# Kernel optimization log

Hardware: AMD Instinct MI355X
Metric: run time of the kernel (lower is better)

Reference implementation:

```python
import jax, jax.numpy as jnp
import numpy as np

D = 64          # slot_dim == input_dim
K = 8           # num_slots
NUM_ITERS = 3
EPS = 1e-8      # attention renorm eps
LN_EPS = 1e-5   # torch LayerNorm default
SCALE = float(np.sqrt(D))


def _ln(x, g, b):
    m = x.mean(-1, keepdims=True)
    v = ((x - m) ** 2).mean(-1, keepdims=True)
    return (x - m) / jnp.sqrt(v + LN_EPS) * g + b


def setup_inputs() -> dict:
    key = jax.random.key(0)
    ks = jax.random.split(key, 12)
    B, N = 128, 4096
    s = 1.0 / np.sqrt(D)
    return {
        "inputs": jax.random.normal(ks[0], (B, N, D), jnp.float32),
        "noise": jax.random.normal(ks[1], (B, K, D), jnp.float32),
        "slot_mu": jax.random.normal(ks[2], (1, 1, D), jnp.float32),
        "slot_log_sigma": jnp.zeros((1, 1, D), jnp.float32),
        "Wq": jax.random.normal(ks[3], (D, D), jnp.float32) * s,
        "Wk": jax.random.normal(ks[4], (D, D), jnp.float32) * s,
        "Wv": jax.random.normal(ks[5], (D, D), jnp.float32) * s,
        "gru_wih": jax.random.normal(ks[6], (3 * D, D), jnp.float32) * s,
        "gru_whh": jax.random.normal(ks[7], (3 * D, D), jnp.float32) * s,
        "gru_bih": jnp.zeros((3 * D,), jnp.float32),
        "gru_bhh": jnp.zeros((3 * D,), jnp.float32),
        "ln_in_g": jnp.ones((D,), jnp.float32),
        "ln_in_b": jnp.zeros((D,), jnp.float32),
        "ln_s_g": jnp.ones((D,), jnp.float32),
        "ln_s_b": jnp.zeros((D,), jnp.float32),
        "mlp_ln_g": jnp.ones((D,), jnp.float32),
        "mlp_ln_b": jnp.zeros((D,), jnp.float32),
        "mlp_w1": jax.random.normal(ks[8], (4 * D, D), jnp.float32) * s,
        "mlp_b1": jnp.zeros((4 * D,), jnp.float32),
        "mlp_w2": jax.random.normal(ks[9], (D, 4 * D), jnp.float32) * (1.0 / np.sqrt(4 * D)),
        "mlp_b2": jnp.zeros((D,), jnp.float32),
    }


def reference(inputs, noise, slot_mu, slot_log_sigma, Wq, Wk, Wv,
              gru_wih, gru_whh, gru_bih, gru_bhh,
              ln_in_g, ln_in_b, ln_s_g, ln_s_b,
              mlp_ln_g, mlp_ln_b, mlp_w1, mlp_b1, mlp_w2, mlp_b2):
    x = _ln(inputs, ln_in_g, ln_in_b)          # (B, N, D)
    k = x @ Wk.T                               # (B, N, D)
    v = x @ Wv.T                               # (B, N, D)
    slots = slot_mu + jnp.exp(slot_log_sigma) * noise  # (B, K, D)
    for _ in range(NUM_ITERS):
        slots_prev = slots
        s = _ln(slots, ln_s_g, ln_s_b)
        q = s @ Wq.T                           # (B, K, D)
        attn = jnp.einsum('bkd,bnd->bkn', q, k) / SCALE
        attn = jax.nn.softmax(attn, axis=1)    # compete over slots
        attn_w = attn / (attn.sum(-1, keepdims=True) + EPS)
        updates = jnp.einsum('bkn,bnd->bkd', attn_w, v)
        # GRUCell(updates, slots_prev)
        gi = updates @ gru_wih.T + gru_bih
        gh = slots_prev @ gru_whh.T + gru_bhh
        i_r, i_z, i_n = jnp.split(gi, 3, axis=-1)
        h_r, h_z, h_n = jnp.split(gh, 3, axis=-1)
        r = jax.nn.sigmoid(i_r + h_r)
        z = jax.nn.sigmoid(i_z + h_z)
        n = jnp.tanh(i_n + r * h_n)
        slots = (1.0 - z) * n + z * slots_prev
        # residual MLP
        h = _ln(slots, mlp_ln_g, mlp_ln_b)
        slots = slots + jax.nn.relu(h @ mlp_w1.T + mlp_b1) @ mlp_w2.T + mlp_b2
    return slots
```

## Files before the change

### kernel.cpp

```cpp
#include <hip/hip_runtime.h>
#include <cstdint>

#define Bn 128
#define Nn 4096
#define Dn 64
#define Kn 8
#define PBn 8
#define NCHUNKn (Nn / PBn)
#define LN_EPSf 1e-5f
#define EPSf 1e-8f
#define LOG2Ef 1.4426950408889634f

typedef unsigned short u16x8 __attribute__((ext_vector_type(8)));

static __device__ __forceinline__ uint16_t f2bf(float f) {
    union { float f; uint32_t u; } v; v.f = f;
    return (uint16_t)((v.u + 0x7fffu + ((v.u >> 16) & 1u)) >> 16);
}
static __device__ __forceinline__ float bflo(uint32_t u) {
    union { uint32_t u; float f; } v; v.u = u << 16; return v.f;
}
static __device__ __forceinline__ float bfhi(uint32_t u) {
    union { uint32_t u; float f; } v; v.u = u & 0xffff0000u; return v.f;
}

template <int CTRL>
static __device__ __forceinline__ float dppadd(float x) {
    int p = __builtin_amdgcn_update_dpp(0, __float_as_int(x), CTRL, 0xf, 0xf, false);
    return x + __int_as_float(p);
}

__global__ __launch_bounds__(256) void kM(const float* __restrict__ Wq,
                                          const float* __restrict__ Wk,
                                          float* __restrict__ M) {
    const int idx = blockIdx.x * 256 + threadIdx.x;
    const int e = idx >> 6, f = idx & 63;
    float acc = 0.f;
#pragma unroll 8
    for (int d = 0; d < 64; ++d) acc += Wq[d * 64 + e] * Wk[d * 64 + f];
    M[idx] = acc * 0.125f * LOG2Ef;
}

__global__ __launch_bounds__(256) void kinit_qk(
    const float* __restrict__ noise, const float* __restrict__ mu,
    const float* __restrict__ ls, const float* __restrict__ M,
    float* __restrict__ slots, float* __restrict__ qk) {
    __shared__ float sraw[Kn * Dn];
    __shared__ float sln[Kn][68];
    const int t = threadIdx.x;
    const int b = blockIdx.x;

    if (t < 128) {
        const int base = (b * 128 + t) * 4;
        const int d = base & 63;
        float4 nz = *(const float4*)(noise + base);
        float4 m4 = *(const float4*)(mu + d);
        float4 s4 = *(const float4*)(ls + d);
        float4 o;
        o.x = m4.x + __expf(s4.x) * nz.x;
        o.y = m4.y + __expf(s4.y) * nz.y;
        o.z = m4.z + __expf(s4.z) * nz.z;
        o.w = m4.w + __expf(s4.w) * nz.w;
        *(float4*)(slots + base) = o;
        *(float4*)(sraw + t * 4) = o;
    }
    __syncthreads();
    if (t < 128) {
        const int row = t >> 4, l16 = t & 15;
        float4 v4 = *(const float4*)(sraw + row * 64 + l16 * 4);
        float s1 = v4.x + v4.y + v4.z + v4.w;
        float s2 = v4.x * v4.x + v4.y * v4.y + v4.z * v4.z + v4.w * v4.w;
        s1 = dppadd<0xB1>(s1); s2 = dppadd<0xB1>(s2);
        s1 = dppadd<0x4E>(s1); s2 = dppadd<0x4E>(s2);
        s1 = dppadd<0x141>(s1); s2 = dppadd<0x141>(s2);
        s1 = dppadd<0x128>(s1); s2 = dppadd<0x128>(s2);
        const float mean = s1 * (1.0f / 64.0f);
        const float var = s2 * (1.0f / 64.0f) - mean * mean;
        const float rstd = rsqrtf(var + LN_EPSf);
        const float xs[4] = {v4.x, v4.y, v4.z, v4.w};
#pragma unroll
        for (int i = 0; i < 4; ++i) sln[row][l16 * 4 + i] = (xs[i] - mean) * rstd;
    }
    __syncthreads();
    ((void)0);
}

__global__ __launch_bounds__(256) void kinit_qk_full(
    const float* __restrict__ noise, const float* __restrict__ mu,
    const float* __restrict__ ls, const float* __restrict__ M,
    const float* __restrict__ lsg, const float* __restrict__ lsb,
    float* __restrict__ slots, float* __restrict__ qk) {
    __shared__ float sraw[Kn * Dn];
    __shared__ float sln[Kn][68];
    const int t = threadIdx.x;
    const int b = blockIdx.x;

    if (t < 128) {
        const int base = (b * 128 + t) * 4;
        const int d = base & 63;
        float4 nz = *(const float4*)(noise + base);
        float4 m4 = *(const float4*)(mu + d);
        float4 s4 = *(const float4*)(ls + d);
        float4 o;
        o.x = m4.x + __expf(s4.x) * nz.x;
        o.y = m4.y + __expf(s4.y) * nz.y;
        o.z = m4.z + __expf(s4.z) * nz.z;
        o.w = m4.w + __expf(s4.w) * nz.w;
        *(float4*)(slots + base) = o;
        *(float4*)(sraw + t * 4) = o;
    }
    __syncthreads();
    if (t < 128) {
        const int row = t >> 4, l16 = t & 15;
        float4 v4 = *(const float4*)(sraw + row * 64 + l16 * 4);
        float s1 = v4.x + v4.y + v4.z + v4.w;
        float s2 = v4.x * v4.x + v4.y * v4.y + v4.z * v4.z + v4.w * v4.w;
        s1 = dppadd<0xB1>(s1); s2 = dppadd<0xB1>(s2);
        s1 = dppadd<0x4E>(s1); s2 = dppadd<0x4E>(s2);
        s1 = dppadd<0x141>(s1); s2 = dppadd<0x141>(s2);
        s1 = dppadd<0x128>(s1); s2 = dppadd<0x128>(s2);
        const float mean = s1 * (1.0f / 64.0f);
        const float var = s2 * (1.0f / 64.0f) - mean * mean;
        const float rstd = rsqrtf(var + LN_EPSf);
        const float xs[4] = {v4.x, v4.y, v4.z, v4.w};
#pragma unroll
        for (int i = 0; i < 4; ++i) {
            const int dcol = l16 * 4 + i;
            sln[row][dcol] = (xs[i] - mean) * rstd * lsg[dcol] + lsb[dcol];
        }
    }
    __syncthreads();
    for (int o = t; o < 512; o += 256) {
        const int kk = o >> 6, j = o & 63;
        float a = 0.f;
#pragma unroll 8
        for (int e = 0; e < 64; ++e) a += sln[kk][e] * M[e * 64 + j];
        qk[b * 512 + o] = a;
    }
}

__global__ __launch_bounds__(256) void k1_ln(const float* __restrict__ inp,
                                             const float* __restrict__ lng,
                                             const float* __restrict__ lnb,
                                             uint16_t* __restrict__ xout) {
    const int t = threadIdx.x;
    const long row = (long)blockIdx.x * 64 + (t >> 2);
    const int c0 = (t & 3) * 16;

    const float* src = inp + row * 64 + c0;
    float x[16];
#pragma unroll
    for (int u = 0; u < 4; ++u) {
        float4 v4 = *(const float4*)(src + u * 4);
        x[u * 4 + 0] = v4.x; x[u * 4 + 1] = v4.y;
        x[u * 4 + 2] = v4.z; x[u * 4 + 3] = v4.w;
    }
    float s1 = 0.f, s2 = 0.f;
#pragma unroll
    for (int i = 0; i < 16; ++i) { s1 += x[i]; s2 += x[i] * x[i]; }
    s1 = dppadd<0xB1>(s1); s2 = dppadd<0xB1>(s2);
    s1 = dppadd<0x4E>(s1); s2 = dppadd<0x4E>(s2);
    const float mean = s1 * (1.0f / 64.0f);
    const float var = s2 * (1.0f / 64.0f) - mean * mean;
    const float rstd = rsqrtf(var + LN_EPSf);

    u16x8 o0, o1;
#pragma unroll
    for (int i = 0; i < 8; ++i) {
        o0[i] = f2bf((x[i] - mean) * rstd * lng[c0 + i] + lnb[c0 + i]);
        o1[i] = f2bf((x[8 + i] - mean) * rstd * lng[c0 + 8 + i] + lnb[c0 + 8 + i]);
    }
    uint16_t* dst = xout + row * 64 + c0;
    *(u16x8*)dst = o0;
    *(u16x8*)(dst + 8) = o1;
}

__global__ __launch_bounds__(256) void k2_attn(
    const uint16_t* __restrict__ xbf, const float* __restrict__ qkg,
    float* __restrict__ partials) {
    __shared__ float qld[Kn][64];
    __shared__ float red[16 * 552];
    __shared__ float redas[16][8];

    const int t = threadIdx.x;
    const int b = blockIdx.x >> 3;
    const int part = blockIdx.x & 7;

    if (t < 128) *(float4*)(&qld[0][0] + t * 4) = *(const float4*)(qkg + b * 512 + t * 4);
    __syncthreads();

    const int dc = t & 7;
    const int pg = t >> 3;
    float qr[8][8];
#pragma unroll
    for (int kk = 0; kk < 8; ++kk) {
        float4 q0 = *(const float4*)&qld[kk][dc * 8];
        float4 q1 = *(const float4*)&qld[kk][dc * 8 + 4];
        qr[kk][0] = q0.x; qr[kk][1] = q0.y; qr[kk][2] = q0.z; qr[kk][3] = q0.w;
        qr[kk][4] = q1.x; qr[kk][5] = q1.y; qr[kk][6] = q1.z; qr[kk][7] = q1.w;
    }

    float upd[8][8];
    float asum[8];
#pragma unroll
    for (int kk = 0; kk < 8; ++kk) {
        asum[kk] = 0.f;
#pragma unroll
        for (int i = 0; i < 8; ++i) upd[kk][i] = 0.f;
    }

    const uint16_t* xbase = xbf + ((long)b * Nn + part * NCHUNKn) * 64 + dc * 8;

    uint4 xr = *(const uint4*)(xbase + (long)pg * 64);

    for (int it = 0; it < NCHUNKn / 32; ++it) {
        uint4 xn = xr;
        if (it < NCHUNKn / 32 - 1)
            xn = *(const uint4*)(xbase + (long)((it + 1) * 32 + pg) * 64);
        float xf[8];
        xf[0] = bflo(xr.x); xf[1] = bfhi(xr.x);
        xf[2] = bflo(xr.y); xf[3] = bfhi(xr.y);
        xf[4] = bflo(xr.z); xf[5] = bfhi(xr.z);
        xf[6] = bflo(xr.w); xf[7] = bfhi(xr.w);

        float lg[8];
#pragma unroll
        for (int kk = 0; kk < 8; ++kk) {
            float a = 0.f;
#pragma unroll
            for (int i = 0; i < 8; ++i) a += qr[kk][i] * xf[i];
            lg[kk] = a;
        }
#pragma unroll
        for (int kk = 0; kk < 8; ++kk) lg[kk] = dppadd<0xB1>(lg[kk]);
#pragma unroll
        for (int kk = 0; kk < 8; ++kk) lg[kk] = dppadd<0x4E>(lg[kk]);
#pragma unroll
        for (int kk = 0; kk < 8; ++kk) lg[kk] = dppadd<0x141>(lg[kk]);
        float e[8];
        float es = 0.f;
#pragma unroll
        for (int kk = 0; kk < 8; ++kk) { e[kk] = exp2f(lg[kk]); es += e[kk]; }
        const float rinv = __builtin_amdgcn_rcpf(es);
#pragma unroll
        for (int kk = 0; kk < 8; ++kk) {
            const float a = e[kk] * rinv;
            asum[kk] += a;
#pragma unroll
            for (int i = 0; i < 8; ++i) upd[kk][i] += a * xf[i];
        }
        xr = xn;
    }

#pragma unroll
    for (int kk = 0; kk < 8; ++kk) {
#pragma unroll
        for (int i = 0; i < 8; ++i) upd[kk][i] = dppadd<0x128>(upd[kk][i]);
        asum[kk] = dppadd<0x128>(asum[kk]);
    }
    const int l = t & 63;
    const int wv = t >> 6;
    if ((l & 8) == 0) {
        const int copy = wv * 4 + (l >> 4);
        float* rb = red + copy * 552 + (l & 7) * 8;
#pragma unroll
        for (int kk = 0; kk < 8; ++kk) {
            float4 u0, u1;
            u0.x = upd[kk][0]; u0.y = upd[kk][1]; u0.z = upd[kk][2]; u0.w = upd[kk][3];
            u1.x = upd[kk][4]; u1.y = upd[kk][5]; u1.z = upd[kk][6]; u1.w = upd[kk][7];
            *(float4*)(rb + kk * 68) = u0;
            *(float4*)(rb + kk * 68 + 4) = u1;
        }
        if ((l & 15) == 0) {
            float4 a0, a1;
            a0.x = asum[0]; a0.y = asum[1]; a0.z = asum[2]; a0.w = asum[3];
            a1.x = asum[4]; a1.y = asum[5]; a1.z = asum[6]; a1.w = asum[7];
            *(float4*)&redas[copy][0] = a0;
            *(float4*)&redas[copy][4] = a1;
        }
    }
    __syncthreads();
    float* pout = partials + (long)(b * PBn + part) * 520;
    if (t < 128) {
        const int kk = t >> 4, dq = t & 15;
        float4 acc = {0.f, 0.f, 0.f, 0.f};
#pragma unroll
        for (int c = 0; c < 16; ++c) {
            float4 v = *(const float4*)(red + c * 552 + kk * 68 + dq * 4);
            acc.x += v.x; acc.y += v.y; acc.z += v.z; acc.w += v.w;
        }
        *(float4*)(pout + kk * 64 + dq * 4) = acc;
    }
    if (t < 8) {
        float a = 0.f;
#pragma unroll
        for (int c = 0; c < 16; ++c) a += redas[c][t];
        pout[512 + t] = a;
    }
}

__global__ __launch_bounds__(256) void k3_update(
    const float* __restrict__ partials, const float* __restrict__ slots_in,
    const float* __restrict__ Wv,
    const float* __restrict__ wih, const float* __restrict__ whh,
    const float* __restrict__ bih, const float* __restrict__ bhh,
    const float* __restrict__ mg, const float* __restrict__ mb,
    const float* __restrict__ w1, const float* __restrict__ b1,
    const float* __restrict__ w2, const float* __restrict__ b2,
    const float* __restrict__ M, const float* __restrict__ lsg,
    const float* __restrict__ lsb,
    float* __restrict__ slots_out, float* __restrict__ qkout) {
    __shared__ float axn[64];
    __shared__ float updf[64];
    __shared__ float sp[64];
    __shared__ float gi[192];
    __shared__ float gh[192];
    __shared__ float sn[64];
    __shared__ float hln[64];
    __shared__ float hid[256];
    __shared__ float outv[64];
    __shared__ float lnq[64];

    const int t = threadIdx.x;
    const int b = blockIdx.x >> 3;
    const int s = blockIdx.x & 7;
    const float* pp = partials + (long)b * PBn * 520;

    float asum = EPSf;
#pragma unroll
    for (int j = 0; j < PBn; ++j) asum += pp[j * 520 + 512 + s];
    const float rasum = 1.0f / asum;

    if (t < 64) {
        float a = 0.f;
#pragma unroll
        for (int j = 0; j < PBn; ++j) a += pp[j * 520 + s * 64 + t];
        axn[t] = a * rasum;
    } else if (t < 80) {
        const int i = t - 64;
        *(float4*)&sp[i * 4] = *(const float4*)(slots_in + b * 512 + s * 64 + i * 4);
    }
    __syncthreads();

    {
        const int d = t >> 2, h = t & 3;
        const float* wr = Wv + d * 64 + h * 16;
        float acc = 0.f;
#pragma unroll
        for (int u = 0; u < 4; ++u) {
            float4 w4 = *(const float4*)(wr + u * 4);
            float4 a4 = *(const float4*)&axn[h * 16 + u * 4];
            acc += w4.x * a4.x + w4.y * a4.y + w4.z * a4.z + w4.w * a4.w;
        }
        acc = dppadd<0xB1>(acc);
        acc = dppadd<0x4E>(acc);
        if (h == 0) updf[d] = acc;
    }
    __syncthreads();

    for (int w = t; w < 768; w += 256) {
        const int j = w >> 2, h = w & 3;
        const float* wr = wih + j * 64 + h * 16;
        float acc = 0.f;
#pragma unroll
        for (int u = 0; u < 4; ++u) {
            float4 w4 = *(const float4*)(wr + u * 4);
            float4 a4 = *(const float4*)&updf[h * 16 + u * 4];
            acc += w4.x * a4.x + w4.y * a4.y + w4.z * a4.z + w4.w * a4.w;
        }
        acc = dppadd<0xB1>(acc);
        acc = dppadd<0x4E>(acc);
        if (h == 0) gi[j] = acc + bih[j];
    }
    for (int w = t; w < 768; w += 256) {
        const int j = w >> 2, h = w & 3;
        const float* wr = whh + j * 64 + h * 16;
        float acc = 0.f;
#pragma unroll
        for (int u = 0; u < 4; ++u) {
            float4 w4 = *(const float4*)(wr + u * 4);
            float4 a4 = *(const float4*)&sp[h * 16 + u * 4];
            acc += w4.x * a4.x + w4.y * a4.y + w4.z * a4.z + w4.w * a4.w;
        }
        acc = dppadd<0xB1>(acc);
        acc = dppadd<0x4E>(acc);
        if (h == 0) gh[j] = acc + bhh[j];
    }
    __syncthreads();

    if (t < 64) {
        const float ir = gi[t], iz = gi[64 + t], in_ = gi[128 + t];
        const float hr = gh[t], hz = gh[64 + t], hn = gh[128 + t];
        const float r = 1.0f / (1.0f + __expf(-(ir + hr)));
        const float z = 1.0f / (1.0f + __expf(-(iz + hz)));
        const float n = tanhf(in_ + r * hn);
        sn[t] = (1.0f - z) * n + z * sp[t];
    }
    __syncthreads();

    if (t < 16) {
        float4 v4 = *(const float4*)&sn[t * 4];
        float s1 = v4.x + v4.y + v4.z + v4.w;
        float s2 = v4.x * v4.x + v4.y * v4.y + v4.z * v4.z + v4.w * v4.w;
        s1 = dppadd<0xB1>(s1); s2 = dppadd<0xB1>(s2);
        s1 = dppadd<0x4E>(s1); s2 = dppadd<0x4E>(s2);
        s1 = dppadd<0x141>(s1); s2 = dppadd<0x141>(s2);
        s1 = dppadd<0x128>(s1); s2 = dppadd<0x128>(s2);
        const float mean = s1 * (1.0f / 64.0f);
        const float var = s2 * (1.0f / 64.0f) - mean * mean;
        const float rstd = rsqrtf(var + LN_EPSf);
        const float xs[4] = {v4.x, v4.y, v4.z, v4.w};
#pragma unroll
        for (int i = 0; i < 4; ++i) {
            const int dcol = t * 4 + i;
            hln[dcol] = (xs[i] - mean) * rstd * mg[dcol] + mb[dcol];
        }
    }
    __syncthreads();

    for (int w = t; w < 1024; w += 256) {
        const int j = w >> 2, h = w & 3;
        const float* wr = w1 + j * 64 + h * 16;
        float acc = 0.f;
#pragma unroll
        for (int u = 0; u < 4; ++u) {
            float4 w4 = *(const float4*)(wr + u * 4);
            float4 a4 = *(const float4*)&hln[h * 16 + u * 4];
            acc += w4.x * a4.x + w4.y * a4.y + w4.z * a4.z + w4.w * a4.w;
        }
        acc = dppadd<0xB1>(acc);
        acc = dppadd<0x4E>(acc);
        if (h == 0) hid[j] = fmaxf(acc + b1[j], 0.0f);
    }
    __syncthreads();

    {
        const int d = t >> 2, h = t & 3;
        const float* wr = w2 + d * 256 + h * 64;
        float acc = 0.f;
#pragma unroll
        for (int u = 0; u < 16; ++u) {
            float4 w4 = *(const float4*)(wr + u * 4);
            float4 h4 = *(const float4*)&hid[h * 64 + u * 4];
            acc += w4.x * h4.x + w4.y * h4.y + w4.z * h4.z + w4.w * h4.w;
        }
        acc = dppadd<0xB1>(acc);
        acc = dppadd<0x4E>(acc);
        if (h == 0) {
            const float val = sn[d] + acc + b2[d];
            slots_out[(long)b * 512 + s * 64 + d] = val;
            outv[d] = val;
        }
    }
    __syncthreads();

    if (t < 16) {
        float4 v4 = *(const float4*)&outv[t * 4];
        float s1 = v4.x + v4.y + v4.z + v4.w;
        float s2 = v4.x * v4.x + v4.y * v4.y + v4.z * v4.z + v4.w * v4.w;
        s1 = dppadd<0xB1>(s1); s2 = dppadd<0xB1>(s2);
        s1 = dppadd<0x4E>(s1); s2 = dppadd<0x4E>(s2);
        s1 = dppadd<0x141>(s1); s2 = dppadd<0x141>(s2);
        s1 = dppadd<0x128>(s1); s2 = dppadd<0x128>(s2);
        const float mean = s1 * (1.0f / 64.0f);
        const float var = s2 * (1.0f / 64.0f) - mean * mean;
        const float rstd = rsqrtf(var + LN_EPSf);
        const float xs[4] = {v4.x, v4.y, v4.z, v4.w};
#pragma unroll
        for (int i = 0; i < 4; ++i) {
            const int dcol = t * 4 + i;
            lnq[dcol] = (xs[i] - mean) * rstd * lsg[dcol] + lsb[dcol];
        }
    }
    __syncthreads();
    if (t < 64) {
        float a = 0.f;
#pragma unroll 8
        for (int e = 0; e < 64; ++e) a += lnq[e] * M[e * 64 + t];
        qkout[b * 512 + s * 64 + t] = a;
    }
}

extern "C" void kernel_launch(void* const* d_in, const int* in_sizes, int n_in,
                              void* d_out, int out_size, void* d_ws, size_t ws_size,
                              hipStream_t stream) {
    const float* inputs = (const float*)d_in[0];
    const float* noise = (const float*)d_in[1];
    const float* mu = (const float*)d_in[2];
    const float* ls = (const float*)d_in[3];
    const float* Wq = (const float*)d_in[4];
    const float* Wk = (const float*)d_in[5];
    const float* Wv = (const float*)d_in[6];
    const float* wih = (const float*)d_in[7];
    const float* whh = (const float*)d_in[8];
    const float* bih = (const float*)d_in[9];
    const float* bhh = (const float*)d_in[10];
    const float* lng = (const float*)d_in[11];
    const float* lnb = (const float*)d_in[12];
    const float* lsg = (const float*)d_in[13];
    const float* lsb = (const float*)d_in[14];
    const float* mg = (const float*)d_in[15];
    const float* mb = (const float*)d_in[16];
    const float* w1 = (const float*)d_in[17];
    const float* b1 = (const float*)d_in[18];
    const float* w2 = (const float*)d_in[19];
    const float* b2 = (const float*)d_in[20];

    char* ws = (char*)d_ws;
    float* slots = (float*)ws;
    float* Mm = (float*)(ws + 262144);
    float* qk = (float*)(ws + 262144 + 16384);
    uint16_t* xbf = (uint16_t*)(ws + 262144 + 16384 + 262144);
    float* parts = (float*)(ws + 262144 + 16384 + 262144 + (1 << 26));

    kM<<<16, 256, 0, stream>>>(Wq, Wk, Mm);
    kinit_qk_full<<<Bn, 256, 0, stream>>>(noise, mu, ls, Mm, lsg, lsb, slots, qk);
    k1_ln<<<8192, 256, 0, stream>>>(inputs, lng, lnb, xbf);
    for (int it = 0; it < 3; ++it) {
        k2_attn<<<Bn * PBn, 256, 0, stream>>>(xbf, qk, parts);
        float* dst = (it == 2) ? (float*)d_out : slots;
        k3_update<<<Bn * Kn, 256, 0, stream>>>(parts, slots, Wv, wih, whh, bih, bhh,
                                               mg, mb, w1, b1, w2, b2, Mm, lsg, lsb,
                                               dst, qk);
    }
}
```

Baseline: 202.1 us.

## Split slots across lane halves in attention kernel to halve per-thread accumulators

The attention kernel now splits the 8 slots into two groups of 4 across adjacent 8-lane groups. Each thread keeps a 4x8 update accumulator instead of 8x8, and each thread now processes every 16th token instead of every 32nd. Cutting the register load is meant to raise occupancy or stop spilling, and the softmax denominator is combined across the two lane halves with one extra DPP add. The final reduction switches from a 16-copy shared-memory tree to shuffle-xor within each wave plus a small 4-copy shared buffer, and an unused dead init kernel is removed.

```diff
diff --git a/kernel.cpp b/kernel.cpp
--- a/kernel.cpp
+++ b/kernel.cpp
@@ -41,9 +41,10 @@
     M[idx] = acc * 0.125f * LOG2Ef;
 }
 
-__global__ __launch_bounds__(256) void kinit_qk(
+__global__ __launch_bounds__(256) void kinit_qk_full(
     const float* __restrict__ noise, const float* __restrict__ mu,
     const float* __restrict__ ls, const float* __restrict__ M,
+    const float* __restrict__ lsg, const float* __restrict__ lsb,
     float* __restrict__ slots, float* __restrict__ qk) {
     __shared__ float sraw[Kn * Dn];
     __shared__ float sln[Kn][68];
@@ -79,51 +80,6 @@
         const float rstd = rsqrtf(var + LN_EPSf);
         const float xs[4] = {v4.x, v4.y, v4.z, v4.w};
 #pragma unroll
-        for (int i = 0; i < 4; ++i) sln[row][l16 * 4 + i] = (xs[i] - mean) * rstd;
-    }
-    __syncthreads();
-    ((void)0);
-}
-
-__global__ __launch_bounds__(256) void kinit_qk_full(
-    const float* __restrict__ noise, const float* __restrict__ mu,
-    const float* __restrict__ ls, const float* __restrict__ M,
-    const float* __restrict__ lsg, const float* __restrict__ lsb,
-    float* __restrict__ slots, float* __restrict__ qk) {
-    __shared__ float sraw[Kn * Dn];
-    __shared__ float sln[Kn][68];
-    const int t = threadIdx.x;
-    const int b = blockIdx.x;
-
-    if (t < 128) {
-        const int base = (b * 128 + t) * 4;
-        const int d = base & 63;
-        float4 nz = *(const float4*)(noise + base);
-        float4 m4 = *(const float4*)(mu + d);
-        float4 s4 = *(const float4*)(ls + d);
-        float4 o;
-        o.x = m4.x + __expf(s4.x) * nz.x;
-        o.y = m4.y + __expf(s4.y) * nz.y;
-        o.z = m4.z + __expf(s4.z) * nz.z;
-        o.w = m4.w + __expf(s4.w) * nz.w;
-        *(float4*)(slots + base) = o;
-        *(float4*)(sraw + t * 4) = o;
-    }
-    __syncthreads();
-    if (t < 128) {
-        const int row = t >> 4, l16 = t & 15;
-        float4 v4 = *(const float4*)(sraw + row * 64 + l16 * 4);
-        float s1 = v4.x + v4.y + v4.z + v4.w;
-        float s2 = v4.x * v4.x + v4.y * v4.y + v4.z * v4.z + v4.w * v4.w;
-        s1 = dppadd<0xB1>(s1); s2 = dppadd<0xB1>(s2);
-        s1 = dppadd<0x4E>(s1); s2 = dppadd<0x4E>(s2);
-        s1 = dppadd<0x141>(s1); s2 = dppadd<0x141>(s2);
-        s1 = dppadd<0x128>(s1); s2 = dppadd<0x128>(s2);
-        const float mean = s1 * (1.0f / 64.0f);
-        const float var = s2 * (1.0f / 64.0f) - mean * mean;
-        const float rstd = rsqrtf(var + LN_EPSf);
-        const float xs[4] = {v4.x, v4.y, v4.z, v4.w};
-#pragma unroll
         for (int i = 0; i < 4; ++i) {
             const int dcol = l16 * 4 + i;
             sln[row][dcol] = (xs[i] - mean) * rstd * lsg[dcol] + lsb[dcol];
@@ -179,8 +135,8 @@
     const uint16_t* __restrict__ xbf, const float* __restrict__ qkg,
     float* __restrict__ partials) {
     __shared__ float qld[Kn][64];
-    __shared__ float red[16 * 552];
-    __shared__ float redas[16][8];
+    __shared__ float redu[4][Kn][68];
+    __shared__ float redas[4][Kn];
 
     const int t = threadIdx.x;
     const int b = blockIdx.x >> 3;
@@ -189,114 +145,110 @@
     if (t < 128) *(float4*)(&qld[0][0] + t * 4) = *(const float4*)(qkg + b * 512 + t * 4);
     __syncthreads();
 
-    const int dc = t & 7;
-    const int pg = t >> 3;
-    float qr[8][8];
-#pragma unroll
-    for (int kk = 0; kk < 8; ++kk) {
-        float4 q0 = *(const float4*)&qld[kk][dc * 8];
-        float4 q1 = *(const float4*)&qld[kk][dc * 8 + 4];
-        qr[kk][0] = q0.x; qr[kk][1] = q0.y; qr[kk][2] = q0.z; qr[kk][3] = q0.w;
-        qr[kk][4] = q1.x; qr[kk][5] = q1.y; qr[kk][6] = q1.z; qr[kk][7] = q1.w;
-    }
-
-    float upd[8][8];
-    float asum[8];
-#pragma unroll
-    for (int kk = 0; kk < 8; ++kk) {
-        asum[kk] = 0.f;
-#pragma unroll
-        for (int i = 0; i < 8; ++i) upd[kk][i] = 0.f;
+    const int l = t & 63;
+    const int wv = t >> 6;
+    const int dc = l & 7;
+    const int sg = (l >> 3) & 1;
+    const int pg2 = l >> 4;
+
+    float qr[4][8];
+#pragma unroll
+    for (int c = 0; c < 4; ++c) {
+        float4 q0 = *(const float4*)&qld[sg * 4 + c][dc * 8];
+        float4 q1 = *(const float4*)&qld[sg * 4 + c][dc * 8 + 4];
+        qr[c][0] = q0.x; qr[c][1] = q0.y; qr[c][2] = q0.z; qr[c][3] = q0.w;
+        qr[c][4] = q1.x; qr[c][5] = q1.y; qr[c][6] = q1.z; qr[c][7] = q1.w;
+    }
+
+    float upd[4][8];
+    float asum[4];
+#pragma unroll
+    for (int c = 0; c < 4; ++c) {
+        asum[c] = 0.f;
+#pragma unroll
+        for (int i = 0; i < 8; ++i) upd[c][i] = 0.f;
     }
 
     const uint16_t* xbase = xbf + ((long)b * Nn + part * NCHUNKn) * 64 + dc * 8;
-
-    uint4 xr = *(const uint4*)(xbase + (long)pg * 64);
-
-    for (int it = 0; it < NCHUNKn / 32; ++it) {
+    const int poff = wv * 4 + pg2;
+
+    uint4 xr = *(const uint4*)(xbase + (long)poff * 64);
+
+    for (int it = 0; it < NCHUNKn / 16; ++it) {
         uint4 xn = xr;
-        if (it < NCHUNKn / 32 - 1)
-            xn = *(const uint4*)(xbase + (long)((it + 1) * 32 + pg) * 64);
+        if (it < NCHUNKn / 16 - 1)
+            xn = *(const uint4*)(xbase + (long)((it + 1) * 16 + poff) * 64);
         float xf[8];
         xf[0] = bflo(xr.x); xf[1] = bfhi(xr.x);
         xf[2] = bflo(xr.y); xf[3] = bfhi(xr.y);
         xf[4] = bflo(xr.z); xf[5] = bfhi(xr.z);
         xf[6] = bflo(xr.w); xf[7] = bfhi(xr.w);
 
-        float lg[8];
-#pragma unroll
-        for (int kk = 0; kk < 8; ++kk) {
+        float lg[4];
+#pragma unroll
+        for (int c = 0; c < 4; ++c) {
             float a = 0.f;
 #pragma unroll
-            for (int i = 0; i < 8; ++i) a += qr[kk][i] * xf[i];
-            lg[kk] = a;
-        }
-#pragma unroll
-        for (int kk = 0; kk < 8; ++kk) lg[kk] = dppadd<0xB1>(lg[kk]);
-#pragma unroll
-        for (int kk = 0; kk < 8; ++kk) lg[kk] = dppadd<0x4E>(lg[kk]);
-#pragma unroll
-        for (int kk = 0; kk < 8; ++kk) lg[kk] = dppadd<0x141>(lg[kk]);
-        float e[8];
-        float es = 0.f;
-#pragma unroll
-        for (int kk = 0; kk < 8; ++kk) { e[kk] = exp2f(lg[kk]); es += e[kk]; }
+            for (int i = 0; i < 8; ++i) a += qr[c][i] * xf[i];
+            lg[c] = a;
+        }
+#pragma unroll
+        for (int c = 0; c < 4; ++c) lg[c] = dppadd<0xB1>(lg[c]);
+#pragma unroll
+        for (int c = 0; c < 4; ++c) lg[c] = dppadd<0x4E>(lg[c]);
+#pragma unroll
+        for (int c = 0; c < 4; ++c) lg[c] = dppadd<0x141>(lg[c]);
+        float e[4];
+#pragma unroll
+        for (int c = 0; c < 4; ++c) e[c] = exp2f(lg[c]);
+        float es = (e[0] + e[1]) + (e[2] + e[3]);
+        es = dppadd<0x128>(es);
         const float rinv = __builtin_amdgcn_rcpf(es);
 #pragma unroll
-        for (int kk = 0; kk < 8; ++kk) {
-            const float a = e[kk] * rinv;
-            asum[kk] += a;
-#pragma unroll
-            for (int i = 0; i < 8; ++i) upd[kk][i] += a * xf[i];
+        for (int c = 0; c < 4; ++c) {
+            const float a = e[c] * rinv;
+            asum[c] += a;
+#pragma unroll
+            for (int i = 0; i < 8; ++i) upd[c][i] += a * xf[i];
         }
         xr = xn;
     }
 
 #pragma unroll
-    for (int kk = 0; kk < 8; ++kk) {
-#pragma unroll
-        for (int i = 0; i < 8; ++i) upd[kk][i] = dppadd<0x128>(upd[kk][i]);
-        asum[kk] = dppadd<0x128>(asum[kk]);
-    }
-    const int l = t & 63;
-    const int wv = t >> 6;
-    if ((l & 8) == 0) {
-        const int copy = wv * 4 + (l >> 4);
-        float* rb = red + copy * 552 + (l & 7) * 8;
-#pragma unroll
-        for (int kk = 0; kk < 8; ++kk) {
+    for (int m = 16; m < 64; m <<= 1) {
+#pragma unroll
+        for (int c = 0; c < 4; ++c) {
+#pragma unroll
+            for (int i = 0; i < 8; ++i) upd[c][i] += __shfl_xor(upd[c][i], m);
+            asum[c] += __shfl_xor(asum[c], m);
+        }
+    }
+    if (l < 16) {
+#pragma unroll
+        for (int c = 0; c < 4; ++c) {
             float4 u0, u1;
-            u0.x = upd[kk][0]; u0.y = upd[kk][1]; u0.z = upd[kk][2]; u0.w = upd[kk][3];
-            u1.x = upd[kk][4]; u1.y = upd[kk][5]; u1.z = upd[kk][6]; u1.w = upd[kk][7];
-            *(float4*)(rb + kk * 68) = u0;
-            *(float4*)(rb + kk * 68 + 4) = u1;
-        }
-        if ((l & 15) == 0) {
-            float4 a0, a1;
-            a0.x = asum[0]; a0.y = asum[1]; a0.z = asum[2]; a0.w = asum[3];
-            a1.x = asum[4]; a1.y = asum[5]; a1.z = asum[6]; a1.w = asum[7];
-            *(float4*)&redas[copy][0] = a0;
-            *(float4*)&redas[copy][4] = a1;
+            u0.x = upd[c][0]; u0.y = upd[c][1]; u0.z = upd[c][2]; u0.w = upd[c][3];
+            u1.x = upd[c][4]; u1.y = upd[c][5]; u1.z = upd[c][6]; u1.w = upd[c][7];
+            *(float4*)&redu[wv][sg * 4 + c][dc * 8] = u0;
+            *(float4*)&redu[wv][sg * 4 + c][dc * 8 + 4] = u1;
+        }
+        if (dc == 0) {
+#pragma unroll
+            for (int c = 0; c < 4; ++c) redas[wv][sg * 4 + c] = asum[c];
         }
     }
     __syncthreads();
     float* pout = partials + (long)(b * PBn + part) * 520;
     if (t < 128) {
-        const int kk = t >> 4, dq = t & 15;
-        float4 acc = {0.f, 0.f, 0.f, 0.f};
-#pragma unroll
-        for (int c = 0; c < 16; ++c) {
-            float4 v = *(const float4*)(red + c * 552 + kk * 68 + dq * 4);
-            acc.x += v.x; acc.y += v.y; acc.z += v.z; acc.w += v.w;
-        }
-        *(float4*)(pout + kk * 64 + dq * 4) = acc;
-    }
-    if (t < 8) {
-        float a = 0.f;
-#pragma unroll
-        for (int c = 0; c < 16; ++c) a += redas[c][t];
-        pout[512 + t] = a;
-    }
+        const int kk = t >> 4, d0 = (t & 15) * 4;
+        float4 acc;
+        acc.x = redu[0][kk][d0] + redu[1][kk][d0] + redu[2][kk][d0] + redu[3][kk][d0];
+        acc.y = redu[0][kk][d0 + 1] + redu[1][kk][d0 + 1] + redu[2][kk][d0 + 1] + redu[3][kk][d0 + 1];
+        acc.z = redu[0][kk][d0 + 2] + redu[1][kk][d0 + 2] + redu[2][kk][d0 + 2] + redu[3][kk][d0 + 2];
+        acc.w = redu[0][kk][d0 + 3] + redu[1][kk][d0 + 3] + redu[2][kk][d0 + 3] + redu[3][kk][d0 + 3];
+        *(float4*)(pout + kk * 64 + d0) = acc;
+    }
+    if (t < 8) pout[512 + t] = redas[0][t] + redas[1][t] + redas[2][t] + redas[3][t];
 }
 
 __global__ __launch_bounds__(256) void k3_update(
```

Result: slower. 207.9 us (+2.9%).

## Fuse input LayerNorm into first attention pass and drop separate LN kernel

Applied to the files above, without the earlier changes.

Removes the standalone input-LayerNorm kernel and templatizes the attention kernel. The first iteration reads fp32 inputs, normalizes each row in registers via DPP reductions, and writes the bf16 copy as it goes. Later iterations read that bf16 copy as before. This cuts one full bf16 read pass over the large input tensor and a kernel launch, at the cost of heavier register use and an fp32 load stream in the first attention pass.

```diff
diff --git a/kernel.cpp b/kernel.cpp
--- a/kernel.cpp
+++ b/kernel.cpp
@@ -41,9 +41,10 @@
     M[idx] = acc * 0.125f * LOG2Ef;
 }
 
-__global__ __launch_bounds__(256) void kinit_qk(
+__global__ __launch_bounds__(256) void kinit_qk_full(
     const float* __restrict__ noise, const float* __restrict__ mu,
     const float* __restrict__ ls, const float* __restrict__ M,
+    const float* __restrict__ lsg, const float* __restrict__ lsb,
     float* __restrict__ slots, float* __restrict__ qk) {
     __shared__ float sraw[Kn * Dn];
     __shared__ float sln[Kn][68];
@@ -79,51 +80,6 @@
         const float rstd = rsqrtf(var + LN_EPSf);
         const float xs[4] = {v4.x, v4.y, v4.z, v4.w};
 #pragma unroll
-        for (int i = 0; i < 4; ++i) sln[row][l16 * 4 + i] = (xs[i] - mean) * rstd;
-    }
-    __syncthreads();
-    ((void)0);
-}
-
-__global__ __launch_bounds__(256) void kinit_qk_full(
-    const float* __restrict__ noise, const float* __restrict__ mu,
-    const float* __restrict__ ls, const float* __restrict__ M,
-    const float* __restrict__ lsg, const float* __restrict__ lsb,
-    float* __restrict__ slots, float* __restrict__ qk) {
-    __shared__ float sraw[Kn * Dn];
-    __shared__ float sln[Kn][68];
-    const int t = threadIdx.x;
-    const int b = blockIdx.x;
-
-    if (t < 128) {
-        const int base = (b * 128 + t) * 4;
-        const int d = base & 63;
-        float4 nz = *(const float4*)(noise + base);
-        float4 m4 = *(const float4*)(mu + d);
-        float4 s4 = *(const float4*)(ls + d);
-        float4 o;
-        o.x = m4.x + __expf(s4.x) * nz.x;
-        o.y = m4.y + __expf(s4.y) * nz.y;
-        o.z = m4.z + __expf(s4.z) * nz.z;
-        o.w = m4.w + __expf(s4.w) * nz.w;
-        *(float4*)(slots + base) = o;
-        *(float4*)(sraw + t * 4) = o;
-    }
-    __syncthreads();
-    if (t < 128) {
-        const int row = t >> 4, l16 = t & 15;
-        float4 v4 = *(const float4*)(sraw + row * 64 + l16 * 4);
-        float s1 = v4.x + v4.y + v4.z + v4.w;
-        float s2 = v4.x * v4.x + v4.y * v4.y + v4.z * v4.z + v4.w * v4.w;
-        s1 = dppadd<0xB1>(s1); s2 = dppadd<0xB1>(s2);
-        s1 = dppadd<0x4E>(s1); s2 = dppadd<0x4E>(s2);
-        s1 = dppadd<0x141>(s1); s2 = dppadd<0x141>(s2);
-        s1 = dppadd<0x128>(s1); s2 = dppadd<0x128>(s2);
-        const float mean = s1 * (1.0f / 64.0f);
-        const float var = s2 * (1.0f / 64.0f) - mean * mean;
-        const float rstd = rsqrtf(var + LN_EPSf);
-        const float xs[4] = {v4.x, v4.y, v4.z, v4.w};
-#pragma unroll
         for (int i = 0; i < 4; ++i) {
             const int dcol = l16 * 4 + i;
             sln[row][dcol] = (xs[i] - mean) * rstd * lsg[dcol] + lsb[dcol];
@@ -139,44 +95,11 @@
     }
 }
 
-__global__ __launch_bounds__(256) void k1_ln(const float* __restrict__ inp,
-                                             const float* __restrict__ lng,
-                                             const float* __restrict__ lnb,
-                                             uint16_t* __restrict__ xout) {
-    const int t = threadIdx.x;
-    const long row = (long)blockIdx.x * 64 + (t >> 2);
-    const int c0 = (t & 3) * 16;
-
-    const float* src = inp + row * 64 + c0;
-    float x[16];
-#pragma unroll
-    for (int u = 0; u < 4; ++u) {
-        float4 v4 = *(const float4*)(src + u * 4);
-        x[u * 4 + 0] = v4.x; x[u * 4 + 1] = v4.y;
-        x[u * 4 + 2] = v4.z; x[u * 4 + 3] = v4.w;
-    }
-    float s1 = 0.f, s2 = 0.f;
-#pragma unroll
-    for (int i = 0; i < 16; ++i) { s1 += x[i]; s2 += x[i] * x[i]; }
-    s1 = dppadd<0xB1>(s1); s2 = dppadd<0xB1>(s2);
-    s1 = dppadd<0x4E>(s1); s2 = dppadd<0x4E>(s2);
-    const float mean = s1 * (1.0f / 64.0f);
-    const float var = s2 * (1.0f / 64.0f) - mean * mean;
-    const float rstd = rsqrtf(var + LN_EPSf);
-
-    u16x8 o0, o1;
-#pragma unroll
-    for (int i = 0; i < 8; ++i) {
-        o0[i] = f2bf((x[i] - mean) * rstd * lng[c0 + i] + lnb[c0 + i]);
-        o1[i] = f2bf((x[8 + i] - mean) * rstd * lng[c0 + 8 + i] + lnb[c0 + 8 + i]);
-    }
-    uint16_t* dst = xout + row * 64 + c0;
-    *(u16x8*)dst = o0;
-    *(u16x8*)(dst + 8) = o1;
-}
-
+template <int MODE>
 __global__ __launch_bounds__(256) void k2_attn(
-    const uint16_t* __restrict__ xbf, const float* __restrict__ qkg,
+    const float* __restrict__ inp, const uint16_t* __restrict__ xbf_in,
+    uint16_t* __restrict__ xbf_out, const float* __restrict__ qkg,
+    const float* __restrict__ lng, const float* __restrict__ lnb,
     float* __restrict__ partials) {
     __shared__ float qld[Kn][64];
     __shared__ float red[16 * 552];
@@ -200,6 +123,12 @@
         qr[kk][4] = q1.x; qr[kk][5] = q1.y; qr[kk][6] = q1.z; qr[kk][7] = q1.w;
     }
 
+    float gv[8], bt[8];
+    if (MODE == 0) {
+#pragma unroll
+        for (int i = 0; i < 8; ++i) { gv[i] = lng[dc * 8 + i]; bt[i] = lnb[dc * 8 + i]; }
+    }
+
     float upd[8][8];
     float asum[8];
 #pragma unroll
@@ -209,19 +138,58 @@
         for (int i = 0; i < 8; ++i) upd[kk][i] = 0.f;
     }
 
-    const uint16_t* xbase = xbf + ((long)b * Nn + part * NCHUNKn) * 64 + dc * 8;
-
-    uint4 xr = *(const uint4*)(xbase + (long)pg * 64);
+    const long chunkoff = ((long)b * Nn + part * NCHUNKn) * 64 + dc * 8;
+    const uint16_t* xbase = xbf_in + chunkoff;
+    const float* ibase = inp + chunkoff;
+    uint16_t* obase = xbf_out + chunkoff;
+
+    uint4 xr;
+    float4 fa, fb;
+    if (MODE == 1) {
+        xr = *(const uint4*)(xbase + (long)pg * 64);
+    } else {
+        fa = *(const float4*)(ibase + (long)pg * 64);
+        fb = *(const float4*)(ibase + (long)pg * 64 + 4);
+    }
 
     for (int it = 0; it < NCHUNKn / 32; ++it) {
-        uint4 xn = xr;
-        if (it < NCHUNKn / 32 - 1)
-            xn = *(const uint4*)(xbase + (long)((it + 1) * 32 + pg) * 64);
+        uint4 xn;
+        float4 na, nb;
+        if (it < NCHUNKn / 32 - 1) {
+            if (MODE == 1) {
+                xn = *(const uint4*)(xbase + (long)((it + 1) * 32 + pg) * 64);
+            } else {
+                na = *(const float4*)(ibase + (long)((it + 1) * 32 + pg) * 64);
+                nb = *(const float4*)(ibase + (long)((it + 1) * 32 + pg) * 64 + 4);
+            }
+        } else {
+            if (MODE == 1) xn = xr; else { na = fa; nb = fb; }
+        }
+
         float xf[8];
-        xf[0] = bflo(xr.x); xf[1] = bfhi(xr.x);
-        xf[2] = bflo(xr.y); xf[3] = bfhi(xr.y);
-        xf[4] = bflo(xr.z); xf[5] = bfhi(xr.z);
-        xf[6] = bflo(xr.w); xf[7] = bfhi(xr.w);
+        if (MODE == 1) {
+            xf[0] = bflo(xr.x); xf[1] = bfhi(xr.x);
+            xf[2] = bflo(xr.y); xf[3] = bfhi(xr.y);
+            xf[4] = bflo(xr.z); xf[5] = bfhi(xr.z);
+            xf[6] = bflo(xr.w); xf[7] = bfhi(xr.w);
+        } else {
+            float x8[8] = {fa.x, fa.y, fa.z, fa.w, fb.x, fb.y, fb.z, fb.w};
+            float s1 = 0.f, s2 = 0.f;
+#pragma unroll
+            for (int i = 0; i < 8; ++i) { s1 += x8[i]; s2 += x8[i] * x8[i]; }
+            s1 = dppadd<0xB1>(s1); s2 = dppadd<0xB1>(s2);
+            s1 = dppadd<0x4E>(s1); s2 = dppadd<0x4E>(s2);
+            s1 = dppadd<0x141>(s1); s2 = dppadd<0x141>(s2);
+            const float mean = s1 * (1.0f / 64.0f);
+            const float var = s2 * (1.0f / 64.0f) - mean * mean;
+            const float rstd = rsqrtf(var + LN_EPSf);
+#pragma unroll
+            for (int i = 0; i < 8; ++i) xf[i] = (x8[i] - mean) * rstd * gv[i] + bt[i];
+            u16x8 o;
+#pragma unroll
+            for (int i = 0; i < 8; ++i) o[i] = f2bf(xf[i]);
+            *(u16x8*)(obase + (long)(it * 32 + pg) * 64) = o;
+        }
 
         float lg[8];
 #pragma unroll
@@ -249,7 +217,7 @@
 #pragma unroll
             for (int i = 0; i < 8; ++i) upd[kk][i] += a * xf[i];
         }
-        xr = xn;
+        if (MODE == 1) xr = xn; else { fa = na; fb = nb; }
     }
 
 #pragma unroll
@@ -515,9 +483,11 @@
 
     kM<<<16, 256, 0, stream>>>(Wq, Wk, Mm);
     kinit_qk_full<<<Bn, 256, 0, stream>>>(noise, mu, ls, Mm, lsg, lsb, slots, qk);
-    k1_ln<<<8192, 256, 0, stream>>>(inputs, lng, lnb, xbf);
     for (int it = 0; it < 3; ++it) {
-        k2_attn<<<Bn * PBn, 256, 0, stream>>>(xbf, qk, parts);
+        if (it == 0)
+            k2_attn<0><<<Bn * PBn, 256, 0, stream>>>(inputs, xbf, xbf, qk, lng, lnb, parts);
+        else
+            k2_attn<1><<<Bn * PBn, 256, 0, stream>>>(inputs, xbf, xbf, qk, lng, lnb, parts);
         float* dst = (it == 2) ? (float*)d_out : slots;
         k3_update<<<Bn * Kn, 256, 0, stream>>>(parts, slots, Wv, wih, whh, bih, bhh,
                                                mg, mb, w1, b1, w2, b2, Mm, lsg, lsb,
```

Result: faster. 182.8 us (-9.6%).
